# Optimization experiments

Hardware: AMD Instinct MI355X
Metric: run time of the kernel (lower is better)

Reference implementation:

```python
import jax, jax.numpy as jnp
import numpy as np

HEAD_DIM = 128
NUM_HEADS = 16
NUM_KV_HEADS = 16
ROPE_MAX_POS = 4096
ROPE_BASE = 10000.0


def _rope_tables(seq_len):
    # cos/sin cached tables: [S, D/2]
    inv_freq = 1.0 / (ROPE_BASE ** (jnp.arange(0, HEAD_DIM, 2, dtype=jnp.float32) / HEAD_DIM))
    t = jnp.arange(seq_len, dtype=jnp.float32)
    freqs = jnp.outer(t, inv_freq)
    return jnp.cos(freqs), jnp.sin(freqs)


def _apply_rope(x, cos, sin):
    # x: [B, S, H, D]; cos/sin: [S, D/2] -> broadcast over heads as [S, 1, D/2]
    orig_dtype = x.dtype
    c = cos[:, None, :]
    s = sin[:, None, :]
    xf = x.astype(jnp.float32)
    x_real, x_im = jnp.split(xf, 2, axis=-1)  # half-split (not interleaved) RoPE
    x_real_e = x_real * c - x_im * s
    x_im_e = x_im * c + x_real * s
    return jnp.concatenate((x_real_e, x_im_e), axis=-1).astype(orig_dtype)


def setup_inputs() -> dict:
    key = jax.random.key(0)
    k1, k2, k3 = jax.random.split(key, 3)
    B, S, H = 1, 4096, 2048
    hidden_states = jax.random.normal(k1, (B, S, H), dtype=jnp.float32)
    # trunc-normal-ish init, std ~ 1/sqrt(fan_in)
    w_qkv = jax.random.normal(k2, ((NUM_HEADS + 2 * NUM_KV_HEADS) * HEAD_DIM, H), dtype=jnp.float32) / jnp.sqrt(jnp.float32(H))
    w_o = jax.random.normal(k3, (H, NUM_HEADS * HEAD_DIM), dtype=jnp.float32) / jnp.sqrt(jnp.float32(NUM_HEADS * HEAD_DIM))
    return {"hidden_states": hidden_states, "w_qkv": w_qkv, "w_o": w_o}


def reference(hidden_states, w_qkv, w_o):
    B, S, _ = hidden_states.shape
    qkv = jnp.einsum('bsh,oh->bso', hidden_states, w_qkv)
    qkv = qkv.reshape(B, S, NUM_HEADS + 2 * NUM_KV_HEADS, HEAD_DIM)
    q = qkv[:, :, :NUM_HEADS]
    k = qkv[:, :, NUM_HEADS:NUM_HEADS + NUM_KV_HEADS]
    v = qkv[:, :, NUM_HEADS + NUM_KV_HEADS:]

    cos, sin = _rope_tables(S)
    q = _apply_rope(q, cos, sin)
    k = _apply_rope(k, cos, sin)

    scale = 1.0 / jnp.sqrt(jnp.float32(HEAD_DIM)).astype(q.dtype)
    # scores: [B, H, Sq, Sk]
    scores = jnp.einsum('bqhd,bkhd->bhqk', q, k) * scale
    causal = jnp.tril(jnp.ones((S, S), dtype=bool))
    scores = jnp.where(causal[None, None], scores, jnp.finfo(scores.dtype).min)
    probs = jax.nn.softmax(scores, axis=-1)
    attn = jnp.einsum('bhqk,bkhd->bqhd', probs, v)
    attn = attn.reshape(B, S, NUM_HEADS * HEAD_DIM)
    return jnp.einsum('bso,ho->bsh', attn, w_o)
```

## Files before the change

### kernel.cpp

```cpp
#include <hip/hip_runtime.h>

typedef __bf16 bf16;
typedef __bf16 bf16x8 __attribute__((ext_vector_type(8)));
typedef __bf16 bf16x4 __attribute__((ext_vector_type(4)));
typedef float f32x4 __attribute__((ext_vector_type(4)));

#define SEQ 4096
#define QKV_LD 6144
#define HNUM 16

__device__ __forceinline__ void async16(const bf16* g, bf16* l) {
    __builtin_amdgcn_global_load_lds((const __attribute__((address_space(1))) void*)g,
                                     (__attribute__((address_space(3))) void*)l, 16, 0, 0);
}

__global__ __launch_bounds__(256) void prep(const float* __restrict__ X, bf16* __restrict__ Xb,
                                            const float* __restrict__ Wq, bf16* __restrict__ Wqb,
                                            const float* __restrict__ Wo, bf16* __restrict__ Wob,
                                            float* __restrict__ T) {
    const int b = blockIdx.x, t = threadIdx.x;
    if (b < 12288) {
        const float* src;
        bf16* dst;
        int off;
        if (b < 4096)       { src = X;  dst = Xb;  off = b; }
        else if (b < 10240) { src = Wq; dst = Wqb; off = b - 4096; }
        else                { src = Wo; dst = Wob; off = b - 10240; }
        int i = (off * 256 + t) * 8;
        f32x4 a = *(const f32x4*)(src + i);
        f32x4 c = *(const f32x4*)(src + i + 4);
        bf16x8 w;
#pragma unroll
        for (int j = 0; j < 4; j++) { w[j] = (bf16)a[j]; w[4 + j] = (bf16)c[j]; }
        *(bf16x8*)(dst + i) = w;
    } else {
        int i = (b - 12288) * 256 + t;
        int s = i >> 6, d = i & 63;
        float inv_freq = powf(10000.0f, -(float)d * (1.0f / 64.0f));
        float ang = (float)s * inv_freq;
        T[2 * i]     = cosf(ang);
        T[2 * i + 1] = sinf(ang);
    }
}


__device__ __forceinline__ bf16x8 ldfrag(const bf16* slot, int row, int qd) {
    int lin  = row * 64 + qd * 16;
    int phys = lin ^ (((lin >> 9) & 1) << 5);
    return *(const bf16x8*)((const char*)slot + phys);
}

#define STG(TT, KKI, BUF)                                                      \
    {                                                                          \
        int tcl = (TT) < NT ? (TT) : NT - 1;                                   \
        const bf16* As = A + (size_t)bm * K + tcl * 64 + (KKI)*32;             \
        const bf16* Bs = B + (size_t)bn * K + tcl * 64 + (KKI)*32;             \
        async16(As + gA,  (bf16*)((char*)&LA[BUF][KKI][0] + lbA));             \
        async16(Bs + gB0, (bf16*)((char*)&LB[BUF][KKI][0] + lbB0));            \
        async16(Bs + gB1, (bf16*)((char*)&LB[BUF][KKI][0] + lbB1));            \
    }

#define PH(KKI, TT, SKK, SBUF, DOVM)                                           \
    {                                                                          \
        bf16x8 aA[4], bB[4];                                                   \
        _Pragma("unroll") for (int i = 0; i < 4; i++)                          \
            aA[i] = ldfrag(&LA[bi][KKI][0], wr * 64 + i * 16 + ln, qd);        \
        _Pragma("unroll") for (int j = 0; j < 4; j++)                          \
            bB[j] = ldfrag(&LB[bi][KKI][0], wc * 64 + j * 16 + ln, qd);        \
        STG(TT, SKK, SBUF);                                                    \
        __builtin_amdgcn_sched_barrier(0);                                     \
        if (DOVM) {                                                            \
            asm volatile("s_waitcnt vmcnt(3)" ::: "memory");                   \
            __builtin_amdgcn_sched_barrier(0);                                 \
        }                                                                      \
        __builtin_amdgcn_s_barrier();                                          \
        __builtin_amdgcn_sched_barrier(0);                                     \
        __builtin_amdgcn_s_setprio(1);                                         \
        _Pragma("unroll") for (int i = 0; i < 4; i++)                          \
            _Pragma("unroll") for (int j = 0; j < 4; j++)                      \
                acc[i][j] = __builtin_amdgcn_mfma_f32_16x16x32_bf16(           \
                    aA[i], bB[j], acc[i][j], 0, 0, 0);                         \
        __builtin_amdgcn_s_setprio(0);                                         \
        __builtin_amdgcn_sched_barrier(0);                                     \
        __builtin_amdgcn_s_barrier();                                          \
        __builtin_amdgcn_sched_barrier(0);                                     \
    }

template <int C_F32>
__global__ __launch_bounds__(512, 2) void gemm128x256(const bf16* __restrict__ A,
                                                      const bf16* __restrict__ B,
                                                      void* __restrict__ Cp,
                                                      int M, int N, int K) {
    __shared__ __align__(16) bf16 LA[2][2][128 * 32];
    __shared__ __align__(16) bf16 LB[2][2][256 * 32];
    const int tid  = threadIdx.x;
    const int wave = tid >> 6, lane = tid & 63;
    const int qd = lane >> 4, ln = lane & 15;
    const int wr = wave >> 2, wc = wave & 3;
    const int bm = blockIdx.x * 128, bn = blockIdx.y * 256;
    const int NT = K >> 6;

    const int PrA  = wave * 1024 + lane * 16;
    const int PrB0 = (2 * wave) * 1024 + lane * 16;
    const int PrB1 = PrB0 + 1024;
    const int LrA  = PrA  ^ (((PrA  >> 9) & 1) << 5);
    const int LrB0 = PrB0 ^ (((PrB0 >> 9) & 1) << 5);
    const int LrB1 = PrB1 ^ (((PrB1 >> 9) & 1) << 5);
    const size_t gA  = (size_t)(LrA  >> 6) * K + ((LrA  & 63) >> 1);
    const size_t gB0 = (size_t)(LrB0 >> 6) * K + ((LrB0 & 63) >> 1);
    const size_t gB1 = (size_t)(LrB1 >> 6) * K + ((LrB1 & 63) >> 1);
    const int lbA = wave * 1024, lbB0 = 2 * wave * 1024, lbB1 = lbB0 + 1024;

    f32x4 acc[4][4] = {};

    STG(0, 0, 0);
    STG(0, 1, 0);
    STG(1, 0, 1);
    __builtin_amdgcn_sched_barrier(0);
    asm volatile("s_waitcnt vmcnt(3)" ::: "memory");
    __builtin_amdgcn_sched_barrier(0);
    __builtin_amdgcn_s_barrier();
    __builtin_amdgcn_sched_barrier(0);

    for (int t = 0; t < NT; ++t) {
        const int bi = t & 1;
        PH(0, t + 1, 1, bi ^ 1, 0)
        PH(1, t + 2, 0, bi,     1)
    }
    asm volatile("s_waitcnt vmcnt(0)" ::: "memory");

    const size_t cb = (size_t)(bm + wr * 64 + qd * 4) * N + (bn + wc * 64 + ln);
#pragma unroll
    for (int mi = 0; mi < 4; mi++)
#pragma unroll
        for (int j = 0; j < 4; j++)
#pragma unroll
            for (int r = 0; r < 4; r++) {
                size_t idx = cb + (size_t)(mi * 16 + r) * N + j * 16;
                if (C_F32) ((float*)Cp)[idx] = acc[mi][j][r];
                else       ((bf16*)Cp)[idx]  = (bf16)acc[mi][j][r];
            }
}

template <int A_F32, int B_F32, int C_F32>
__global__ __launch_bounds__(256) void gemm_nt(const void* __restrict__ Ap,
                                               const void* __restrict__ Bp,
                                               void* __restrict__ Cp,
                                               int M, int N, int K) {
    __shared__ __align__(16) bf16 sA[128 * 32];
    __shared__ __align__(16) bf16 sB[128 * 32];
    const int tid  = threadIdx.x;
    const int wave = tid >> 6, lane = tid & 63;
    const int qd = lane >> 4, ln = lane & 15;
    const int bm = blockIdx.x * 128, bn = blockIdx.y * 128;
    const int wm = (wave >> 1) * 64, wn = (wave & 1) * 64;

    const int srow = wave * 16 + (lane >> 2);
    const int scol = (lane & 3) * 8;
    const size_t rowoff = (size_t)srow * K + scol;
    const size_t rowskip = (size_t)64 * K;

    const bf16* Ab = (const bf16*)Ap + (size_t)bm * K + rowoff;
    const bf16* Bb = (const bf16*)Bp + (size_t)bn * K + rowoff;
    const float* Af = (const float*)Ap + (size_t)bm * K + rowoff;
    const float* Bf = (const float*)Bp + (size_t)bn * K + rowoff;
    bf16* sAd0 = &sA[(wave * 16) * 32];
    bf16* sAd1 = &sA[(64 + wave * 16) * 32];
    bf16* sBd0 = &sB[(wave * 16) * 32];
    bf16* sBd1 = &sB[(64 + wave * 16) * 32];
    bf16* sAw0 = &sA[srow * 32 + scol];
    bf16* sAw1 = &sA[(64 + srow) * 32 + scol];
    bf16* sBw0 = &sB[srow * 32 + scol];
    bf16* sBw1 = &sB[(64 + srow) * 32 + scol];

    f32x4 acc[4][4] = {};
    for (int k0 = 0; k0 < K; k0 += 32) {
        if (A_F32) {
            f32x4 u0 = *(const f32x4*)(Af + k0);
            f32x4 u1 = *(const f32x4*)(Af + k0 + 4);
            f32x4 u2 = *(const f32x4*)(Af + rowskip + k0);
            f32x4 u3 = *(const f32x4*)(Af + rowskip + k0 + 4);
            bf16x8 w0, w1;
#pragma unroll
            for (int i = 0; i < 4; i++) { w0[i] = (bf16)u0[i]; w0[4 + i] = (bf16)u1[i];
                                          w1[i] = (bf16)u2[i]; w1[4 + i] = (bf16)u3[i]; }
            *(bf16x8*)sAw0 = w0;
            *(bf16x8*)sAw1 = w1;
        } else {
            async16(Ab + k0, sAd0);
            async16(Ab + rowskip + k0, sAd1);
        }
        if (B_F32) {
            f32x4 u0 = *(const f32x4*)(Bf + k0);
            f32x4 u1 = *(const f32x4*)(Bf + k0 + 4);
            f32x4 u2 = *(const f32x4*)(Bf + rowskip + k0);
            f32x4 u3 = *(const f32x4*)(Bf + rowskip + k0 + 4);
            bf16x8 w0, w1;
#pragma unroll
            for (int i = 0; i < 4; i++) { w0[i] = (bf16)u0[i]; w0[4 + i] = (bf16)u1[i];
                                          w1[i] = (bf16)u2[i]; w1[4 + i] = (bf16)u3[i]; }
            *(bf16x8*)sBw0 = w0;
            *(bf16x8*)sBw1 = w1;
        } else {
            async16(Bb + k0, sBd0);
            async16(Bb + rowskip + k0, sBd1);
        }
        __syncthreads();
        bf16x8 af[4], bfr[4];
#pragma unroll
        for (int i = 0; i < 4; i++)
            af[i] = *(const bf16x8*)&sA[(wm + i * 16 + ln) * 32 + qd * 8];
#pragma unroll
        for (int j = 0; j < 4; j++)
            bfr[j] = *(const bf16x8*)&sB[(wn + j * 16 + ln) * 32 + qd * 8];
#pragma unroll
        for (int i = 0; i < 4; i++)
#pragma unroll
            for (int j = 0; j < 4; j++)
                acc[i][j] = __builtin_amdgcn_mfma_f32_16x16x32_bf16(af[i], bfr[j], acc[i][j], 0, 0, 0);
        __syncthreads();
    }
    const size_t cbase = (size_t)(bm + wm + qd * 4) * N + (bn + wn + ln);
#pragma unroll
    for (int i = 0; i < 4; i++)
#pragma unroll
        for (int j = 0; j < 4; j++)
#pragma unroll
            for (int r = 0; r < 4; r++) {
                size_t idx = cbase + (size_t)(i * 16 + r) * N + j * 16;
                if (C_F32) ((float*)Cp)[idx] = acc[i][j][r];
                else       ((bf16*)Cp)[idx] = (bf16)acc[i][j][r];
            }
}

__global__ __launch_bounds__(256) void rope_tv(bf16* __restrict__ QKV,
                                               const float* __restrict__ T,
                                               bf16* __restrict__ VT) {
    __shared__ bf16 tl[64][65];
    const int b = blockIdx.x, t = threadIdx.x;
    if (b < 4096) {
        const int s  = b;
        const int hh = t >> 3;
        const int d0 = (t & 7) * 8;
        bf16* p = QKV + (size_t)s * QKV_LD + hh * 128 + d0;
        bf16x8 x0 = *(const bf16x8*)(p);
        bf16x8 x1 = *(const bf16x8*)(p + 64);
        const float2* Tb = (const float2*)T + (size_t)s * 64 + d0;
        bf16x8 y0, y1;
#pragma unroll
        for (int e = 0; e < 8; e++) {
            float2 cs = Tb[e];
            float a = (float)x0[e], c = (float)x1[e];
            y0[e] = (bf16)(a * cs.x - c * cs.y);
            y1[e] = (bf16)(c * cs.x + a * cs.y);
        }
        *(bf16x8*)(p)      = y0;
        *(bf16x8*)(p + 64) = y1;
    } else {
        const int b2 = b - 4096;
        const int s0 = (b2 & 63) * 64;
        const int d0 = (b2 >> 6) * 64;
        const int r = t >> 3, c = t & 7;
#pragma unroll
        for (int u = 0; u < 2; u++) {
            bf16x8 v = *(const bf16x8*)(QKV + (size_t)(s0 + u * 32 + r) * QKV_LD + 4096 + d0 + c * 8);
#pragma unroll
            for (int e = 0; e < 8; e++) tl[u * 32 + r][c * 8 + e] = v[e];
        }
        __syncthreads();
#pragma unroll
        for (int u = 0; u < 2; u++) {
            bf16x8 w;
#pragma unroll
            for (int e = 0; e < 8; e++) w[e] = tl[c * 8 + e][u * 32 + r];
            *(bf16x8*)(VT + (size_t)(d0 + u * 32 + r) * SEQ + s0 + c * 8) = w;
        }
    }
}

__global__ __launch_bounds__(256) void rope_k_inline(bf16* __restrict__ QKV) {
    const int s  = blockIdx.x;
    const int t  = threadIdx.x;
    const int hh = (blockIdx.y << 2) + (t >> 6);
    const int d  = t & 63;
    bf16* p = QKV + (size_t)s * QKV_LD + hh * 128 + d;
    float x0 = (float)p[0];
    float x1 = (float)p[64];
    float inv_freq = powf(10000.0f, -(float)d * (1.0f / 64.0f));
    float ang = (float)s * inv_freq;
    float c = cosf(ang), sn = sinf(ang);
    p[0]  = (bf16)(x0 * c - x1 * sn);
    p[64] = (bf16)(x1 * c + x0 * sn);
}

template <int USE_VT>
__global__ __launch_bounds__(256, 2) void flash_attn(const bf16* __restrict__ QKV,
                                                     const bf16* __restrict__ VT,
                                                     bf16* __restrict__ O) {
    __shared__ __align__(16) bf16 sK[64 * 128];
    __shared__ __align__(16) bf16 sV[128 * 64];
    __shared__ __align__(16) bf16 sP[4][32 * 64];
    const int tid  = threadIdx.x;
    const int wave = tid >> 6, lane = tid & 63;
    const int qd = lane >> 4, ln = lane & 15;
    const int h  = blockIdx.x;
    const int y  = blockIdx.y;
    const int qtile = (y < 16) ? (31 - y) : (y - 16);
    const int qw0 = qtile * 128 + wave * 32;
    const int nkv = 2 * qtile + 2;
    const float scale = 0.08838834764831843f;

    bf16x8 Qf[2][4];
#pragma unroll
    for (int qt = 0; qt < 2; qt++) {
        const bf16* Qg = QKV + (size_t)(qw0 + qt * 16 + ln) * QKV_LD + h * 128;
#pragma unroll
        for (int ks = 0; ks < 4; ks++) {
            bf16x8 q8 = *(const bf16x8*)(Qg + ks * 32 + qd * 8);
#pragma unroll
            for (int e = 0; e < 8; e++) q8[e] = (bf16)((float)q8[e] * scale);
            Qf[qt][ks] = q8;
        }
    }

    f32x4 Oacc[2][8] = {};
    float l_i[2] = {0.0f, 0.0f};

    const int krow = tid >> 4;
    const int kblk = tid & 15;
    const int vrow = tid >> 3;
    const int vblk = tid & 7;
    const int vd   = tid & 127;
    const int vh   = tid >> 7;
    const bf16* Kg  = QKV + 2048 + h * 128;
    const bf16* Vg  = QKV + 4096 + h * 128;
    const bf16* VTg = VT + (size_t)h * 128 * SEQ;

    bf16x8 Kpre[4], Vpre[4];
#pragma unroll
    for (int rr = 0; rr < 4; rr++)
        Kpre[rr] = *(const bf16x8*)(Kg + (size_t)(rr * 16 + krow) * QKV_LD + kblk * 8);
    if (USE_VT) {
#pragma unroll
        for (int u = 0; u < 4; u++)
            Vpre[u] = *(const bf16x8*)(VTg + (size_t)(u * 32 + vrow) * SEQ + vblk * 8);
    } else {
#pragma unroll
        for (int u = 0; u < 4; u++)
#pragma unroll
            for (int j = 0; j < 8; j++)
                Vpre[u][j] = Vg[(size_t)(vh * 32 + u * 8 + j) * QKV_LD + vd];
    }

    for (int kt = 0; kt < nkv; kt++) {
        const int kbase = kt * 64;
#pragma unroll
        for (int rr = 0; rr < 4; rr++) {
            int kv = rr * 16 + krow;
            *(bf16x8*)&sK[kv * 128 + ((kblk ^ (kv & 7)) * 8)] = Kpre[rr];
        }
        if (USE_VT) {
#pragma unroll
            for (int u = 0; u < 4; u++) {
                int d = u * 32 + vrow;
                *(bf16x8*)&sV[d * 64 + ((vblk ^ (d & 7)) * 8)] = Vpre[u];
            }
        } else {
#pragma unroll
            for (int u = 0; u < 4; u++)
                *(bf16x8*)&sV[vd * 64 + (((vh * 4 + u) ^ (vd & 7)) * 8)] = Vpre[u];
        }
        __syncthreads();
        if (kt + 1 < nkv) {
            const int nb = kbase + 64;
#pragma unroll
            for (int rr = 0; rr < 4; rr++)
                Kpre[rr] = *(const bf16x8*)(Kg + (size_t)(nb + rr * 16 + krow) * QKV_LD + kblk * 8);
            if (USE_VT) {
#pragma unroll
                for (int u = 0; u < 4; u++)
                    Vpre[u] = *(const bf16x8*)(VTg + (size_t)(u * 32 + vrow) * SEQ + nb + vblk * 8);
            } else {
#pragma unroll
                for (int u = 0; u < 4; u++)
#pragma unroll
                    for (int j = 0; j < 8; j++)
                        Vpre[u][j] = Vg[(size_t)(nb + vh * 32 + u * 8 + j) * QKV_LD + vd];
            }
        }
        if (kbase <= qw0 + 31) {
            f32x4 Sacc[2][4] = {};
#pragma unroll
            for (int ks = 0; ks < 4; ks++)
#pragma unroll
                for (int j = 0; j < 4; j++) {
                    bf16x8 af = *(const bf16x8*)&sK[(j * 16 + ln) * 128 + (((ks * 4 + qd) ^ (ln & 7)) * 8)];
                    Sacc[0][j] = __builtin_amdgcn_mfma_f32_16x16x32_bf16(af, Qf[0][ks], Sacc[0][j], 0, 0, 0);
                    Sacc[1][j] = __builtin_amdgcn_mfma_f32_16x16x32_bf16(af, Qf[1][ks], Sacc[1][j], 0, 0, 0);
                }
#pragma unroll
            for (int qt = 0; qt < 2; qt++) {
                const int qs = qw0 + qt * 16;
                if (kbase + 63 > qs) {
#pragma unroll
                    for (int j = 0; j < 4; j++)
#pragma unroll
                        for (int r = 0; r < 4; r++)
                            if (kbase + j * 16 + qd * 4 + r > qs + ln) Sacc[qt][j][r] = -1e30f;
                }
                float psum = 0.0f;
#pragma unroll
                for (int j = 0; j < 4; j++) {
                    bf16x4 p4;
#pragma unroll
                    for (int r = 0; r < 4; r++) {
                        float p = __expf(Sacc[qt][j][r]);
                        psum += p;
                        p4[r] = (bf16)p;
                    }
                    int blk = (j * 2 + (qd >> 1)) ^ (ln & 7);
                    *(bf16x4*)&sP[wave][(qt * 16 + ln) * 64 + blk * 8 + (qd & 1) * 4] = p4;
                }
                psum += __shfl_xor(psum, 16);
                psum += __shfl_xor(psum, 32);
                l_i[qt] += psum;
            }
#pragma unroll
            for (int ks = 0; ks < 2; ks++) {
                bf16x8 pf0 = *(const bf16x8*)&sP[wave][(0 * 16 + ln) * 64 + (((ks * 4 + qd) ^ (ln & 7)) * 8)];
                bf16x8 pf1 = *(const bf16x8*)&sP[wave][(1 * 16 + ln) * 64 + (((ks * 4 + qd) ^ (ln & 7)) * 8)];
#pragma unroll
                for (int dt = 0; dt < 8; dt++) {
                    bf16x8 vf = *(const bf16x8*)&sV[(dt * 16 + ln) * 64 + (((ks * 4 + qd) ^ (ln & 7)) * 8)];
                    Oacc[0][dt] = __builtin_amdgcn_mfma_f32_16x16x32_bf16(pf0, vf, Oacc[0][dt], 0, 0, 0);
                    Oacc[1][dt] = __builtin_amdgcn_mfma_f32_16x16x32_bf16(pf1, vf, Oacc[1][dt], 0, 0, 0);
                }
            }
        }
        __syncthreads();
    }
#pragma unroll
    for (int qt = 0; qt < 2; qt++) {
        float linv[4];
#pragma unroll
        for (int r = 0; r < 4; r++)
            linv[r] = 1.0f / __shfl(l_i[qt], (lane & 48) | (qd * 4 + r));
        bf16* Ob = O + (size_t)(qw0 + qt * 16 + qd * 4) * 2048 + h * 128 + ln;
#pragma unroll
        for (int dt = 0; dt < 8; dt++)
#pragma unroll
            for (int r = 0; r < 4; r++)
                Ob[(size_t)r * 2048 + dt * 16] = (bf16)(Oacc[qt][dt][r] * linv[r]);
    }
}

extern "C" void kernel_launch(void* const* d_in, const int* in_sizes, int n_in,
                              void* d_out, int out_size, void* d_ws, size_t ws_size,
                              hipStream_t stream) {
    const float* X    = (const float*)d_in[0];
    const float* Wqkv = (const float*)d_in[1];
    const float* Wo   = (const float*)d_in[2];
    float* out = (float*)d_out;
    bf16* QKV = (bf16*)d_ws;
    bf16* ATT = QKV + (size_t)4096 * 6144;

    const size_t nX = (size_t)4096 * 2048, nWq = (size_t)6144 * 2048, nWo = (size_t)2048 * 2048;
    const size_t need = (nX * 3 + nWq * 2 + nWo) * 2 + nX * 2;

    if (ws_size >= need) {
        bf16* Xb  = ATT + nX;
        bf16* Wqb = Xb + nX;
        bf16* Wob = Wqb + nWq;
        bf16*  VT  = Xb;
        float* Tab = (float*)ATT;
        prep<<<13312, 256, 0, stream>>>(X, Xb, Wqkv, Wqb, Wo, Wob, Tab);
        gemm128x256<0><<<dim3(32, 24), 512, 0, stream>>>(Xb, Wqb, QKV, 4096, 6144, 2048);
        rope_tv<<<6144, 256, 0, stream>>>(QKV, Tab, VT);
        flash_attn<1><<<dim3(HNUM, 32), 256, 0, stream>>>(QKV, VT, ATT);
        gemm128x256<1><<<dim3(32, 8), 512, 0, stream>>>(ATT, Wob, out, 4096, 2048, 2048);
    } else {
        gemm_nt<1, 1, 0><<<dim3(32, 48), 256, 0, stream>>>(X, Wqkv, QKV, 4096, 6144, 2048);
        rope_k_inline<<<dim3(4096, 8), 256, 0, stream>>>(QKV);
        flash_attn<0><<<dim3(HNUM, 32), 256, 0, stream>>>(QKV, (const bf16*)nullptr, ATT);
        gemm_nt<0, 1, 1><<<dim3(32, 16), 256, 0, stream>>>(ATT, Wo, out, 4096, 2048, 2048);
    }
}
```

Before: 416.4 us.

## Use 256x256 QKV GEMM with fused RoPE epilogue and XCD-aware tile remap

Replaces the 128x256 QKV projection GEMM with a new 256x256-tile kernel whose epilogue applies RoPE to the Q and K columns directly from accumulators. This removes the separate RoPE read-modify-write pass over QKV and leaves a standalone V transpose kernel. Both GEMMs also get a block index remap that groups tiles per XCD for better L2 locality. Flash attention gains s_setprio around its MFMA sections. The larger tile raises register and LDS pressure, and the fused epilogue does uncoalesced scalar bf16 stores with table reads.

```diff
diff --git a/kernel.cpp b/kernel.cpp
--- a/kernel.cpp
+++ b/kernel.cpp
@@ -43,8 +43,137 @@
     }
 }
 
-
 __device__ __forceinline__ bf16x8 ldfrag(const bf16* slot, int row, int qd) {
+    int lin  = row * 64 + qd * 16;
+    int phys = lin ^ (((lin >> 9) & 1) << 5);
+    return *(const bf16x8*)((const char*)slot + phys);
+}
+
+#define STAGE2(SG, SGR0, STT, SKK, SBUF, SMAT)                                  \
+    {                                                                           \
+        int tcl = (STT) < NT ? (STT) : NT - 1;                                  \
+        const bf16* gsrc = (SG) + (size_t)(SGR0)*K + tcl * 64 + (SKK)*32;       \
+        bf16* sl = &LDS[SBUF][SMAT][SKK][0];                                    \
+        async16(gsrc + g0, (bf16*)((char*)sl + lb0));                           \
+        async16(gsrc + g1, (bf16*)((char*)sl + lb1));                           \
+    }
+
+#define PHASE(QM, KKI, LOADB, SG, SGR0, STT, SKK, SBUF, SMAT, DOVM)             \
+    {                                                                           \
+        if (LOADB) {                                                            \
+            _Pragma("unroll") for (int j = 0; j < 4; j++)                       \
+                bB[j] = ldfrag(&LDS[bi][1][KKI][0],                             \
+                               (wc >> 1) * 128 + (wc & 1) * 32 +                \
+                                   (j & 1) * 16 + (j >> 1) * 64 + ln, qd);      \
+        }                                                                       \
+        bf16x8 aA[4];                                                           \
+        _Pragma("unroll") for (int i = 0; i < 4; i++)                           \
+            aA[i] = ldfrag(&LDS[bi][0][KKI][0],                                 \
+                           wr * 128 + (QM)*64 + i * 16 + ln, qd);               \
+        STAGE2(SG, SGR0, STT, SKK, SBUF, SMAT);                                 \
+        __builtin_amdgcn_sched_barrier(0);                                      \
+        if (DOVM) {                                                             \
+            asm volatile("s_waitcnt vmcnt(4)" ::: "memory");                    \
+            __builtin_amdgcn_sched_barrier(0);                                  \
+        }                                                                       \
+        __builtin_amdgcn_s_barrier();                                           \
+        __builtin_amdgcn_sched_barrier(0);                                      \
+        __builtin_amdgcn_s_setprio(1);                                          \
+        _Pragma("unroll") for (int i = 0; i < 4; i++)                           \
+            _Pragma("unroll") for (int j = 0; j < 4; j++)                       \
+                acc[(QM)*4 + i][j] = __builtin_amdgcn_mfma_f32_16x16x32_bf16(   \
+                    aA[i], bB[j], acc[(QM)*4 + i][j], 0, 0, 0);                 \
+        __builtin_amdgcn_s_setprio(0);                                          \
+        __builtin_amdgcn_sched_barrier(0);                                      \
+        __builtin_amdgcn_s_barrier();                                           \
+        __builtin_amdgcn_sched_barrier(0);                                      \
+    }
+
+template <int ROPE>
+__global__ __launch_bounds__(512, 2) void gemm256_nt(const bf16* __restrict__ A,
+                                                     const bf16* __restrict__ B,
+                                                     bf16* __restrict__ C,
+                                                     int M, int N, int K,
+                                                     const float* __restrict__ T) {
+    __shared__ __align__(16) bf16 LDS[2][2][2][256 * 32];
+    const int tid  = threadIdx.x;
+    const int wave = tid >> 6, lane = tid & 63;
+    const int qd = lane >> 4, ln = lane & 15;
+    const int wr = wave >> 2, wc = wave & 3;
+    const int lin = blockIdx.x + gridDim.x * blockIdx.y;
+    const int nwg = gridDim.x * gridDim.y;
+    const int job = (lin & 7) * (nwg >> 3) + (lin >> 3);
+    const int bm = (job % gridDim.x) * 256;
+    const int bn = (job / gridDim.x) * 256;
+    const int NT = K >> 6;
+
+    const int seg0 = wave * 2, seg1 = seg0 + 1;
+    const int Pr0 = seg0 * 1024 + lane * 16;
+    const int Pr1 = seg1 * 1024 + lane * 16;
+    const int Lr0 = Pr0 ^ (((Pr0 >> 9) & 1) << 5);
+    const int Lr1 = Pr1 ^ (((Pr1 >> 9) & 1) << 5);
+    const size_t g0 = (size_t)(Lr0 >> 6) * K + ((Lr0 & 63) >> 1);
+    const size_t g1 = (size_t)(Lr1 >> 6) * K + ((Lr1 & 63) >> 1);
+    const int lb0 = seg0 * 1024, lb1 = seg1 * 1024;
+
+    f32x4 acc[8][4] = {};
+
+    STAGE2(A, bm, 0, 0, 0, 0);
+    STAGE2(B, bn, 0, 0, 0, 1);
+    STAGE2(A, bm, 0, 1, 0, 0);
+    STAGE2(B, bn, 0, 1, 0, 1);
+    STAGE2(A, bm, 1, 0, 1, 0);
+    STAGE2(B, bn, 1, 0, 1, 1);
+    __builtin_amdgcn_sched_barrier(0);
+    asm volatile("s_waitcnt vmcnt(4)" ::: "memory");
+    __builtin_amdgcn_sched_barrier(0);
+    __builtin_amdgcn_s_barrier();
+    __builtin_amdgcn_sched_barrier(0);
+
+    for (int t = 0; t < NT; ++t) {
+        const int bi = t & 1;
+        bf16x8 bB[4];
+        PHASE(0, 0, 1, A, bm, t + 1, 1, bi ^ 1, 0, 0)
+        PHASE(1, 0, 0, B, bn, t + 1, 1, bi ^ 1, 1, 0)
+        PHASE(0, 1, 1, A, bm, t + 2, 0, bi,     0, 0)
+        PHASE(1, 1, 0, B, bn, t + 2, 0, bi,     1, 1)
+    }
+    asm volatile("s_waitcnt vmcnt(0)" ::: "memory");
+
+    const int colb = bn + (wc >> 1) * 128 + (wc & 1) * 32 + ln;
+    if (ROPE && bn < 4096) {
+        const float2* T2 = (const float2*)T;
+        const int d0 = (wc & 1) * 32 + ln;
+#pragma unroll
+        for (int mi = 0; mi < 8; mi++)
+#pragma unroll
+            for (int r = 0; r < 4; r++) {
+                int row = bm + wr * 128 + mi * 16 + qd * 4 + r;
+                float2 cs0 = T2[(size_t)row * 64 + d0];
+                float2 cs1 = T2[(size_t)row * 64 + d0 + 16];
+                float a0 = acc[mi][0][r], b0 = acc[mi][2][r];
+                float a1 = acc[mi][1][r], b1 = acc[mi][3][r];
+                size_t o = (size_t)row * N + colb;
+                C[o]      = (bf16)(a0 * cs0.x - b0 * cs0.y);
+                C[o + 64] = (bf16)(b0 * cs0.x + a0 * cs0.y);
+                C[o + 16] = (bf16)(a1 * cs1.x - b1 * cs1.y);
+                C[o + 80] = (bf16)(b1 * cs1.x + a1 * cs1.y);
+            }
+    } else {
+#pragma unroll
+        for (int mi = 0; mi < 8; mi++)
+#pragma unroll
+            for (int r = 0; r < 4; r++) {
+                size_t o = (size_t)(bm + wr * 128 + mi * 16 + qd * 4 + r) * N + colb;
+                C[o]      = (bf16)acc[mi][0][r];
+                C[o + 16] = (bf16)acc[mi][1][r];
+                C[o + 64] = (bf16)acc[mi][2][r];
+                C[o + 80] = (bf16)acc[mi][3][r];
+            }
+    }
+}
+
+__device__ __forceinline__ bf16x8 ldfragB(const bf16* slot, int row, int qd) {
     int lin  = row * 64 + qd * 16;
     int phys = lin ^ (((lin >> 9) & 1) << 5);
     return *(const bf16x8*)((const char*)slot + phys);
@@ -64,9 +193,9 @@
     {                                                                          \
         bf16x8 aA[4], bB[4];                                                   \
         _Pragma("unroll") for (int i = 0; i < 4; i++)                          \
-            aA[i] = ldfrag(&LA[bi][KKI][0], wr * 64 + i * 16 + ln, qd);        \
+            aA[i] = ldfragB(&LA[bi][KKI][0], wr * 64 + i * 16 + ln, qd);       \
         _Pragma("unroll") for (int j = 0; j < 4; j++)                          \
-            bB[j] = ldfrag(&LB[bi][KKI][0], wc * 64 + j * 16 + ln, qd);        \
+            bB[j] = ldfragB(&LB[bi][KKI][0], wc * 64 + j * 16 + ln, qd);       \
         STG(TT, SKK, SBUF);                                                    \
         __builtin_amdgcn_sched_barrier(0);                                     \
         if (DOVM) {                                                            \
@@ -97,7 +226,11 @@
     const int wave = tid >> 6, lane = tid & 63;
     const int qd = lane >> 4, ln = lane & 15;
     const int wr = wave >> 2, wc = wave & 3;
-    const int bm = blockIdx.x * 128, bn = blockIdx.y * 256;
+    const int lin = blockIdx.x + gridDim.x * blockIdx.y;
+    const int nwg = gridDim.x * gridDim.y;
+    const int job = (lin & 7) * (nwg >> 3) + (lin >> 3);
+    const int bm = (job % gridDim.x) * 128;
+    const int bn = (job / gridDim.x) * 256;
     const int NT = K >> 6;
 
     const int PrA  = wave * 1024 + lane * 16;
@@ -233,48 +366,26 @@
             }
 }
 
-__global__ __launch_bounds__(256) void rope_tv(bf16* __restrict__ QKV,
-                                               const float* __restrict__ T,
-                                               bf16* __restrict__ VT) {
+__global__ __launch_bounds__(256) void transpose_v(const bf16* __restrict__ QKV,
+                                                   bf16* __restrict__ VT) {
     __shared__ bf16 tl[64][65];
-    const int b = blockIdx.x, t = threadIdx.x;
-    if (b < 4096) {
-        const int s  = b;
-        const int hh = t >> 3;
-        const int d0 = (t & 7) * 8;
-        bf16* p = QKV + (size_t)s * QKV_LD + hh * 128 + d0;
-        bf16x8 x0 = *(const bf16x8*)(p);
-        bf16x8 x1 = *(const bf16x8*)(p + 64);
-        const float2* Tb = (const float2*)T + (size_t)s * 64 + d0;
-        bf16x8 y0, y1;
-#pragma unroll
-        for (int e = 0; e < 8; e++) {
-            float2 cs = Tb[e];
-            float a = (float)x0[e], c = (float)x1[e];
-            y0[e] = (bf16)(a * cs.x - c * cs.y);
-            y1[e] = (bf16)(c * cs.x + a * cs.y);
-        }
-        *(bf16x8*)(p)      = y0;
-        *(bf16x8*)(p + 64) = y1;
-    } else {
-        const int b2 = b - 4096;
-        const int s0 = (b2 & 63) * 64;
-        const int d0 = (b2 >> 6) * 64;
-        const int r = t >> 3, c = t & 7;
-#pragma unroll
-        for (int u = 0; u < 2; u++) {
-            bf16x8 v = *(const bf16x8*)(QKV + (size_t)(s0 + u * 32 + r) * QKV_LD + 4096 + d0 + c * 8);
-#pragma unroll
-            for (int e = 0; e < 8; e++) tl[u * 32 + r][c * 8 + e] = v[e];
-        }
-        __syncthreads();
-#pragma unroll
-        for (int u = 0; u < 2; u++) {
-            bf16x8 w;
-#pragma unroll
-            for (int e = 0; e < 8; e++) w[e] = tl[c * 8 + e][u * 32 + r];
-            *(bf16x8*)(VT + (size_t)(d0 + u * 32 + r) * SEQ + s0 + c * 8) = w;
-        }
+    const int b2 = blockIdx.x;
+    const int s0 = (b2 & 63) * 64;
+    const int d0 = (b2 >> 6) * 64;
+    const int r = threadIdx.x >> 3, c = threadIdx.x & 7;
+#pragma unroll
+    for (int u = 0; u < 2; u++) {
+        bf16x8 v = *(const bf16x8*)(QKV + (size_t)(s0 + u * 32 + r) * QKV_LD + 4096 + d0 + c * 8);
+#pragma unroll
+        for (int e = 0; e < 8; e++) tl[u * 32 + r][c * 8 + e] = v[e];
+    }
+    __syncthreads();
+#pragma unroll
+    for (int u = 0; u < 2; u++) {
+        bf16x8 w;
+#pragma unroll
+        for (int e = 0; e < 8; e++) w[e] = tl[c * 8 + e][u * 32 + r];
+        *(bf16x8*)(VT + (size_t)(d0 + u * 32 + r) * SEQ + s0 + c * 8) = w;
     }
 }
 
@@ -390,6 +501,7 @@
         }
         if (kbase <= qw0 + 31) {
             f32x4 Sacc[2][4] = {};
+            __builtin_amdgcn_s_setprio(1);
 #pragma unroll
             for (int ks = 0; ks < 4; ks++)
 #pragma unroll
@@ -398,6 +510,7 @@
                     Sacc[0][j] = __builtin_amdgcn_mfma_f32_16x16x32_bf16(af, Qf[0][ks], Sacc[0][j], 0, 0, 0);
                     Sacc[1][j] = __builtin_amdgcn_mfma_f32_16x16x32_bf16(af, Qf[1][ks], Sacc[1][j], 0, 0, 0);
                 }
+            __builtin_amdgcn_s_setprio(0);
 #pragma unroll
             for (int qt = 0; qt < 2; qt++) {
                 const int qs = qw0 + qt * 16;
@@ -425,6 +538,7 @@
                 psum += __shfl_xor(psum, 32);
                 l_i[qt] += psum;
             }
+            __builtin_amdgcn_s_setprio(1);
 #pragma unroll
             for (int ks = 0; ks < 2; ks++) {
                 bf16x8 pf0 = *(const bf16x8*)&sP[wave][(0 * 16 + ln) * 64 + (((ks * 4 + qd) ^ (ln & 7)) * 8)];
@@ -436,6 +550,7 @@
                     Oacc[1][dt] = __builtin_amdgcn_mfma_f32_16x16x32_bf16(pf1, vf, Oacc[1][dt], 0, 0, 0);
                 }
             }
+            __builtin_amdgcn_s_setprio(0);
         }
         __syncthreads();
     }
@@ -474,8 +589,8 @@
         bf16*  VT  = Xb;
         float* Tab = (float*)ATT;
         prep<<<13312, 256, 0, stream>>>(X, Xb, Wqkv, Wqb, Wo, Wob, Tab);
-        gemm128x256<0><<<dim3(32, 24), 512, 0, stream>>>(Xb, Wqb, QKV, 4096, 6144, 2048);
-        rope_tv<<<6144, 256, 0, stream>>>(QKV, Tab, VT);
+        gemm256_nt<1><<<dim3(16, 24), 512, 0, stream>>>(Xb, Wqb, QKV, 4096, 6144, 2048, Tab);
+        transpose_v<<<2048, 256, 0, stream>>>(QKV, VT);
         flash_attn<1><<<dim3(HNUM, 32), 256, 0, stream>>>(QKV, VT, ATT);
         gemm128x256<1><<<dim3(32, 8), 512, 0, stream>>>(ATT, Wob, out, 4096, 2048, 2048);
     } else {
```

Result: no change. 417.8 us (+0.3%).
